# Performance work log

Measured on AMD Instinct MI355X. Metric: run time of the kernel, lower is better.

## Reference

```python
import jax, jax.numpy as jnp
import numpy as np

B, T, C, H = 8, 2048, 768, 64  # batch, block_size, n_embd, head_size

def setup_inputs() -> dict:
    key = jax.random.key(0)
    kx, kk, kq, kv = jax.random.split(key, 4)
    x = jax.random.normal(kx, (B, T, C), dtype=jnp.float32)
    Wk = jax.random.normal(kk, (C, H), dtype=jnp.float32) * (C ** -0.5)
    Wq = jax.random.normal(kq, (C, H), dtype=jnp.float32) * (C ** -0.5)
    Wv = jax.random.normal(kv, (C, H), dtype=jnp.float32) * (C ** -0.5)
    return {"x": x, "Wk": Wk, "Wq": Wq, "Wv": Wv}

def reference(x, Wk, Wq, Wv):
    # single causal self-attention head (dropout in eval mode = identity)
    k = jnp.einsum('btc,ch->bth', x, Wk)  # [B,T,H]
    q = jnp.einsum('btc,ch->bth', x, Wq)
    v = jnp.einsum('btc,ch->bth', x, Wv)
    scale = jnp.asarray(k.shape[-1], x.dtype) ** -0.5
    wei = jnp.einsum('bth,bsh->bts', q, k) * scale  # [B,T,T]
    t = x.shape[1]
    causal = jnp.tril(jnp.ones((t, t), dtype=bool))
    wei = jnp.where(causal[None, :, :], wei, jnp.asarray(-jnp.inf, wei.dtype))
    wei = jax.nn.softmax(wei, axis=-1)
    out = jnp.einsum('bts,bsh->bth', wei, v)  # [B,T,H]
    return out
```

## Files before the change

### kernel.cpp

```cpp
#include <hip/hip_runtime.h>
#include <hip/hip_bf16.h>

typedef __attribute__((ext_vector_type(8))) short short8;
typedef __attribute__((ext_vector_type(4))) float f32x4;

#define B_  8
#define T_  2048
#define C_  768
#define H_  64
#define M_  (B_ * T_)

#define GLDS16(g, l) __builtin_amdgcn_global_load_lds(                        \
    (const __attribute__((address_space(1))) void*)(g),                       \
    (__attribute__((address_space(3))) void*)(l), 16, 0, 0)

static __device__ __forceinline__ unsigned short f2bf(float f) {
    __hip_bfloat16 h = __float2bfloat16(f);
    return *reinterpret_cast<unsigned short*>(&h);
}

static __device__ __forceinline__ short8 make_frag(const unsigned short* p0, const unsigned short* p1) {
    const ushort4 a = *reinterpret_cast<const ushort4*>(p0);
    const ushort4 b = *reinterpret_cast<const ushort4*>(p1);
    short8 r;
    r[0] = (short)a.x; r[1] = (short)a.y; r[2] = (short)a.z; r[3] = (short)a.w;
    r[4] = (short)b.x; r[5] = (short)b.y; r[6] = (short)b.z; r[7] = (short)b.w;
    return r;
}

static __device__ __forceinline__ int swz(int row, int u) {
    return row * 64 + ((((u) >> 3) ^ (row & 7)) << 3) + (u & 7);
}

static __device__ __forceinline__ int fragoff(int k) {
    const int half = k >> 5;
    const int kk   = k & 31;
    const int c    = half * 4 + ((kk >> 2) & 3);
    const int p    = (kk & 3) + ((kk & 16) >> 2);
    return c * 8 + p;
}

#define LOG2E_SCALE 0.18033688011112042f

__global__ __launch_bounds__(256) void prep_w(
    const float* __restrict__ Wq, const float* __restrict__ Wk, const float* __restrict__ Wv,
    unsigned short* __restrict__ Wt) {

    const int t   = threadIdx.x;
    const int mat = blockIdx.x / 48;
    const int kb  = blockIdx.x % 48;
    const int h   = t & 63;
    const int k0  = (kb * 4 + (t >> 6)) * 4;

    const float* Ws = (mat == 0) ? Wq : (mat == 1) ? Wk : Wv;
    const float sc  = (mat == 0) ? LOG2E_SCALE : 1.f;
    ushort4 o;
    o.x = f2bf(Ws[(size_t)(k0 + 0) * H_ + h] * sc);
    o.y = f2bf(Ws[(size_t)(k0 + 1) * H_ + h] * sc);
    o.z = f2bf(Ws[(size_t)(k0 + 2) * H_ + h] * sc);
    o.w = f2bf(Ws[(size_t)(k0 + 3) * H_ + h] * sc);
    *reinterpret_cast<ushort4*>(&Wt[(size_t)(mat * 64 + h) * C_ + k0]) = o;
}

__global__ __launch_bounds__(256) void proj_kernel(
    const float* __restrict__ x, const unsigned short* __restrict__ Wt,
    unsigned short* __restrict__ qkv) {

    __shared__ unsigned short Als[2][8192];

    const int tid = threadIdx.x;
    const int w   = tid >> 6;
    const int l   = tid & 63;
    const int lg  = l >> 4;
    const int lc  = l & 15;
    const int row0 = blockIdx.x * 64;

    const int sr   = tid >> 2;
    const int so   = tid & 3;
    const int srt  = sr >> 4;
    const int sr15 = sr & 15;
    const int sbase = (so * 16 + (sr15 ^ so)) * 8;

    f32x4 acc[4][3];
#pragma unroll
    for (int rt = 0; rt < 4; ++rt)
#pragma unroll
        for (int ct = 0; ct < 3; ++ct) acc[rt][ct] = (f32x4)0.f;

    const unsigned short* bbase[3];
#pragma unroll
    for (int ct = 0; ct < 3; ++ct)
        bbase[ct] = Wt + (size_t)(w * 48 + ct * 16 + lc) * C_ + lg * 8;

    const float* xrow = x + (size_t)(row0 + sr) * C_ + so * 8;

    float4 fa[4][2];
#pragma unroll
    for (int jj = 0; jj < 4; ++jj) {
        fa[jj][0] = *reinterpret_cast<const float4*>(xrow + jj * 32);
        fa[jj][1] = *reinterpret_cast<const float4*>(xrow + jj * 32 + 4);
    }

#pragma unroll
    for (int c = 0; c < 6; ++c) {
#pragma unroll
        for (int jj = 0; jj < 4; ++jj) {
            short8 v;
            v[0] = (short)f2bf(fa[jj][0].x); v[1] = (short)f2bf(fa[jj][0].y);
            v[2] = (short)f2bf(fa[jj][0].z); v[3] = (short)f2bf(fa[jj][0].w);
            v[4] = (short)f2bf(fa[jj][1].x); v[5] = (short)f2bf(fa[jj][1].y);
            v[6] = (short)f2bf(fa[jj][1].z); v[7] = (short)f2bf(fa[jj][1].w);
            *reinterpret_cast<short8*>(&Als[c & 1][(srt * 4 + jj) * 512 + sbase]) = v;
        }
        if (c < 5) {
#pragma unroll
            for (int jj = 0; jj < 4; ++jj) {
                fa[jj][0] = *reinterpret_cast<const float4*>(xrow + (c + 1) * 128 + jj * 32);
                fa[jj][1] = *reinterpret_cast<const float4*>(xrow + (c + 1) * 128 + jj * 32 + 4);
            }
        }
        __syncthreads();
#pragma unroll
        for (int kk = 0; kk < 4; ++kk) {
            short8 bcur[3];
#pragma unroll
            for (int ct = 0; ct < 3; ++ct)
                bcur[ct] = *reinterpret_cast<const short8*>(bbase[ct] + c * 128 + kk * 32);
            short8 af[4];
#pragma unroll
            for (int rt = 0; rt < 4; ++rt)
                af[rt] = *reinterpret_cast<const short8*>(
                    &Als[c & 1][(rt * 4 + kk) * 512 + (lg * 16 + (lc ^ lg)) * 8]);
#pragma unroll
            for (int rt = 0; rt < 4; ++rt)
#pragma unroll
                for (int ct = 0; ct < 3; ++ct)
                    acc[rt][ct] = __builtin_amdgcn_mfma_f32_16x16x32_bf16(af[rt], bcur[ct], acc[rt][ct], 0, 0, 0);
        }
    }

    unsigned short* Qd   = qkv;
    unsigned short* Kimg = qkv + (size_t)M_ * H_;
    unsigned short* Vimg = qkv + (size_t)2 * M_ * H_;
    const size_t g12 = (size_t)blockIdx.x << 12;
#pragma unroll
    for (int ct = 0; ct < 3; ++ct) {
        const int col = w * 48 + ct * 16 + lc;
        const int mat = col >> 6;
        const int h   = col & 63;
        const int foh = fragoff(h);
#pragma unroll
        for (int rt = 0; rt < 4; ++rt)
#pragma unroll
            for (int j = 0; j < 4; ++j) {
                const int s6 = rt * 16 + lg * 4 + j;
                const unsigned short v = f2bf(acc[rt][ct][j]);
                if (mat == 0)      Qd[(size_t)(row0 + s6) * H_ + h] = v;
                else if (mat == 1) Kimg[g12 + swz(s6, foh)] = v;
                else               Vimg[g12 + swz(h, fragoff(s6))] = v;
            }
    }
}

#define SEG_FLOATS 4224

template<int SEG>
static __device__ __forceinline__ int segs_per_batch() { return SEG == 32 ? 32 : 80; }

template<int SEG>
static __device__ __forceinline__ void decode_seg(int r, int& qt, int& seg) {
    if (SEG == 32) { qt = r; seg = 0; return; }
    if (r < 8)       { qt = r;                seg = 0; }
    else if (r < 24) { qt = 8  + (r - 8) / 2; seg = (r - 8) & 1; }
    else if (r < 48) { qt = 16 + (r - 24) / 3; seg = (r - 24) % 3; }
    else             { qt = 24 + (r - 48) / 4; seg = (r - 48) & 3; }
}

template<int SEG>
static __device__ __forceinline__ int seg_prefix(int qt) {
    if (SEG == 32) return qt;
    if (qt < 8)  return qt;
    if (qt < 16) return 8  + 2 * (qt - 8);
    if (qt < 24) return 24 + 3 * (qt - 16);
    return 48 + 4 * (qt - 24);
}

template<int SEG>
__global__ __launch_bounds__(256) void attn_partial(
    const unsigned short* __restrict__ qkv, float* __restrict__ part,
    float* __restrict__ out) {

    const int spb = segs_per_batch<SEG>();
    const int b   = blockIdx.x / spb;
    const int rr  = spb - 1 - (blockIdx.x % spb);
    int qt, seg;
    decode_seg<SEG>(rr, qt, seg);

    const int tid = threadIdx.x;
    const int w  = tid >> 6;
    const int l  = tid & 63;
    const int lg = l >> 4;
    const int lc = l & 15;

    __shared__ unsigned short Kls[2][4096];
    __shared__ unsigned short Vls[2][4096];

    const unsigned short* Qg = qkv;
    const unsigned short* Kg = qkv + (size_t)M_ * H_;
    const unsigned short* Vg = qkv + (size_t)2 * M_ * H_;

    const unsigned short* qrow = Qg + (size_t)(b * T_ + qt * 64 + w * 16 + lc) * H_;
    short8 qf[2];
#pragma unroll
    for (int ks = 0; ks < 2; ++ks)
        qf[ks] = make_frag(qrow + ks * 32 + lg * 4, qrow + ks * 32 + lg * 4 + 16);

    float mval = -1e30f, lsum = 0.f;
    f32x4 oT[4];
#pragma unroll
    for (int t = 0; t < 4; ++t) oT[t] = (f32x4)0.f;

    const int q_glob = qt * 64 + w * 16 + lc;

    const int kv_beg = seg * SEG;
    const int kv_end = min(kv_beg + SEG, qt + 1);

    const int go = w * 1024 + l * 8;

    auto stage = [&](int buf, int kv) {
        const size_t tb = ((size_t)(b * 32 + kv)) << 12;
        const unsigned short* kt = Kg + tb;
        const unsigned short* vt = Vg + tb;
        GLDS16(kt + go,       &Kls[buf][w * 1024]);
        GLDS16(kt + go + 512, &Kls[buf][w * 1024 + 512]);
        GLDS16(vt + go,       &Vls[buf][w * 1024]);
        GLDS16(vt + go + 512, &Vls[buf][w * 1024 + 512]);
    };

    stage(0, kv_beg);
    int cur = 0;

    for (int kv = kv_beg; kv < kv_end; ++kv) {
        const bool more = (kv + 1 < kv_end);
        __builtin_amdgcn_s_barrier();
        asm volatile("" ::: "memory");
        if (more) {
            stage(cur ^ 1, kv + 1);
            asm volatile("s_waitcnt vmcnt(4)" ::: "memory");
        } else {
            asm volatile("s_waitcnt vmcnt(0)" ::: "memory");
        }
        __builtin_amdgcn_s_barrier();
        asm volatile("" ::: "memory");

        const unsigned short* Kc = Kls[cur];
        const unsigned short* Vc = Vls[cur];

        f32x4 sT[4];
#pragma unroll
        for (int st = 0; st < 4; ++st) {
            f32x4 accs = (f32x4)0.f;
#pragma unroll
            for (int ks = 0; ks < 2; ++ks) {
                const short8 kf = *reinterpret_cast<const short8*>(
                    &Kc[swz(st * 16 + lc, (ks * 4 + lg) * 8)]);
                accs = __builtin_amdgcn_mfma_f32_16x16x32_bf16(kf, qf[ks], accs, 0, 0, 0);
            }
            sT[st] = accs;
        }

        float p[4][4];
#pragma unroll
        for (int st = 0; st < 4; ++st)
#pragma unroll
            for (int r = 0; r < 4; ++r)
                p[st][r] = sT[st][r];

        if (kv == qt) {
#pragma unroll
            for (int st = 0; st < 4; ++st)
#pragma unroll
                for (int r = 0; r < 4; ++r)
                    if ((kv * 64 + st * 16 + lg * 4 + r) > q_glob) p[st][r] = -1e30f;
        }

        float pm[4];
#pragma unroll
        for (int st = 0; st < 4; ++st)
            pm[st] = fmaxf(fmaxf(p[st][0], p[st][1]), fmaxf(p[st][2], p[st][3]));
        float pmax = fmaxf(fmaxf(pm[0], pm[1]), fmaxf(pm[2], pm[3]));
        pmax = fmaxf(pmax, __shfl_xor(pmax, 16));
        pmax = fmaxf(pmax, __shfl_xor(pmax, 32));

        if (!__all(pmax <= mval)) {
            const float mnew  = fmaxf(mval, pmax);
            const float alpha = exp2f(mval - mnew);
            mval = mnew;
            lsum *= alpha;
#pragma unroll
            for (int ht = 0; ht < 4; ++ht) oT[ht] *= alpha;
        }

        float ps[4];
#pragma unroll
        for (int st = 0; st < 4; ++st) {
#pragma unroll
            for (int r = 0; r < 4; ++r)
                p[st][r] = exp2f(p[st][r] - mval);
            ps[st] = (p[st][0] + p[st][1]) + (p[st][2] + p[st][3]);
        }
        float srow = (ps[0] + ps[1]) + (ps[2] + ps[3]);
        srow += __shfl_xor(srow, 16);
        srow += __shfl_xor(srow, 32);
        lsum += srow;

        short8 pb[2];
#pragma unroll
        for (int ks = 0; ks < 2; ++ks) {
#pragma unroll
            for (int r = 0; r < 4; ++r) {
                pb[ks][r]     = (short)f2bf(p[2 * ks][r]);
                pb[ks][r + 4] = (short)f2bf(p[2 * ks + 1][r]);
            }
        }

#pragma unroll
        for (int ks = 0; ks < 2; ++ks) {
#pragma unroll
            for (int ht = 0; ht < 4; ++ht) {
                const short8 vf = *reinterpret_cast<const short8*>(
                    &Vc[swz(ht * 16 + lc, (ks * 4 + lg) * 8)]);
                oT[ht] = __builtin_amdgcn_mfma_f32_16x16x32_bf16(vf, pb[ks], oT[ht], 0, 0, 0);
            }
        }
        cur ^= 1;
    }

    const int nseg = (SEG == 32) ? 1 : (qt / 8 + 1);
    if (nseg == 1) {
        const float inv = 1.f / lsum;
        float* op = out + (size_t)(b * T_ + q_glob) * H_;
#pragma unroll
        for (int ht = 0; ht < 4; ++ht) {
            f32x4 v = oT[ht] * inv;
            *reinterpret_cast<f32x4*>(&op[ht * 16 + lg * 4]) = v;
        }
    } else {
        float* base = part + (size_t)(b * spb + seg_prefix<SEG>(qt) + seg) * SEG_FLOATS;
#pragma unroll
        for (int ht = 0; ht < 4; ++ht)
            *reinterpret_cast<f32x4*>(&base[(w * 16 + lc) * 64 + ht * 16 + lg * 4]) = oT[ht];
        if (lg == 0) {
            base[4096 + w * 16 + lc] = mval;
            base[4160 + w * 16 + lc] = lsum;
        }
    }
}

__global__ __launch_bounds__(256) void attn_merge8(
    const float* __restrict__ part, float* __restrict__ out) {

    const int b  = blockIdx.x / 24;
    const int qt = 8 + blockIdx.x % 24;
    const int nseg = qt / 8 + 1;
    const float* base0 = part + (size_t)(b * 80 + seg_prefix<8>(qt)) * SEG_FLOATS;

    const int tid = threadIdx.x;
    const int row = tid >> 2;
    const int c0  = (tid & 3) * 16;

    float M = -1e30f;
    for (int s = 0; s < nseg; ++s)
        M = fmaxf(M, base0[(size_t)s * SEG_FLOATS + 4096 + row]);

    float L = 0.f;
    f32x4 acc[4];
#pragma unroll
    for (int k = 0; k < 4; ++k) acc[k] = (f32x4)0.f;

    for (int s = 0; s < nseg; ++s) {
        const float* sb = base0 + (size_t)s * SEG_FLOATS;
        const float wsc = exp2f(sb[4096 + row] - M);
        L += sb[4160 + row] * wsc;
#pragma unroll
        for (int k = 0; k < 4; ++k) {
            const f32x4 ov = *reinterpret_cast<const f32x4*>(&sb[row * 64 + c0 + 4 * k]);
            acc[k] += ov * wsc;
        }
    }
    const float inv = 1.f / L;
    float* op = out + (size_t)(b * T_ + qt * 64 + row) * H_ + c0;
#pragma unroll
    for (int k = 0; k < 4; ++k)
        *reinterpret_cast<f32x4*>(&op[4 * k]) = acc[k] * inv;
}

extern "C" void kernel_launch(void* const* d_in, const int* in_sizes, int n_in,
                              void* d_out, int out_size, void* d_ws, size_t ws_size,
                              hipStream_t stream) {
    const float* x  = (const float*)d_in[0];
    const float* Wk = (const float*)d_in[1];
    const float* Wq = (const float*)d_in[2];
    const float* Wv = (const float*)d_in[3];

    const size_t qkvB = (size_t)3 * M_ * H_ * 2;
    const size_t WtB  = (size_t)3 * H_ * C_ * 2;
    unsigned short* qkv = (unsigned short*)d_ws;
    unsigned short* Wt  = (unsigned short*)((char*)d_ws + qkvB);
    float* part = (float*)((char*)d_ws + qkvB + WtB);
    float* out  = (float*)d_out;

    prep_w<<<dim3(144), dim3(256), 0, stream>>>(Wq, Wk, Wv, Wt);
    proj_kernel<<<dim3(M_ / 64), dim3(256), 0, stream>>>(x, Wt, qkv);

    const size_t need8 = qkvB + WtB + (size_t)(B_ * 80) * SEG_FLOATS * 4;
    if (ws_size >= need8) {
        attn_partial<8><<<dim3(B_ * 80), dim3(256), 0, stream>>>(qkv, part, out);
        attn_merge8<<<dim3(B_ * 24), dim3(256), 0, stream>>>(part, out);
    } else {
        attn_partial<32><<<dim3(B_ * 32), dim3(256), 0, stream>>>(qkv, part, out);
    }
}
```

Measured before the change: 56.12 us.

## Process KV tiles in pairs and stage QKV projection output through LDS

```diff
diff --git a/kernel.cpp b/kernel.cpp
--- a/kernel.cpp
+++ b/kernel.cpp
@@ -139,10 +139,8 @@
         }
     }
 
-    unsigned short* Qd   = qkv;
-    unsigned short* Kimg = qkv + (size_t)M_ * H_;
-    unsigned short* Vimg = qkv + (size_t)2 * M_ * H_;
-    const size_t g12 = (size_t)blockIdx.x << 12;
+    __syncthreads();
+    unsigned short* Ls = &Als[0][0];
 #pragma unroll
     for (int ct = 0; ct < 3; ++ct) {
         const int col = w * 48 + ct * 16 + lc;
@@ -155,10 +153,27 @@
             for (int j = 0; j < 4; ++j) {
                 const int s6 = rt * 16 + lg * 4 + j;
                 const unsigned short v = f2bf(acc[rt][ct][j]);
-                if (mat == 0)      Qd[(size_t)(row0 + s6) * H_ + h] = v;
-                else if (mat == 1) Kimg[g12 + swz(s6, foh)] = v;
-                else               Vimg[g12 + swz(h, fragoff(s6))] = v;
-            }
+                if (mat == 0)      Ls[s6 * 64 + h] = v;
+                else if (mat == 1) Ls[4096 + swz(s6, foh)] = v;
+                else               Ls[8192 + swz(h, fragoff(s6))] = v;
+            }
+    }
+    __syncthreads();
+
+    unsigned short* Qd   = qkv;
+    unsigned short* Kimg = qkv + (size_t)M_ * H_;
+    unsigned short* Vimg = qkv + (size_t)2 * M_ * H_;
+    const size_t g12 = (size_t)blockIdx.x << 12;
+    const int o = tid * 8;
+#pragma unroll
+    for (int s = 0; s < 2; ++s) {
+        const int off = s * 2048 + o;
+        *reinterpret_cast<short8*>(&Qd[(size_t)row0 * 64 + off]) =
+            *reinterpret_cast<const short8*>(&Ls[off]);
+        *reinterpret_cast<short8*>(&Kimg[g12 + off]) =
+            *reinterpret_cast<const short8*>(&Ls[4096 + off]);
+        *reinterpret_cast<short8*>(&Vimg[g12 + off]) =
+            *reinterpret_cast<const short8*>(&Ls[8192 + off]);
     }
 }
 
@@ -202,8 +217,8 @@
     const int lg = l >> 4;
     const int lc = l & 15;
 
-    __shared__ unsigned short Kls[2][4096];
-    __shared__ unsigned short Vls[2][4096];
+    __shared__ unsigned short Kls[2][2][4096];
+    __shared__ unsigned short Vls[2][2][4096];
 
     const unsigned short* Qg = qkv;
     const unsigned short* Kg = qkv + (size_t)M_ * H_;
@@ -224,71 +239,89 @@
 
     const int kv_beg = seg * SEG;
     const int kv_end = min(kv_beg + SEG, qt + 1);
+    const int npair  = (kv_end - kv_beg + 1) >> 1;
 
     const int go = w * 1024 + l * 8;
 
-    auto stage = [&](int buf, int kv) {
-        const size_t tb = ((size_t)(b * 32 + kv)) << 12;
-        const unsigned short* kt = Kg + tb;
-        const unsigned short* vt = Vg + tb;
-        GLDS16(kt + go,       &Kls[buf][w * 1024]);
-        GLDS16(kt + go + 512, &Kls[buf][w * 1024 + 512]);
-        GLDS16(vt + go,       &Vls[buf][w * 1024]);
-        GLDS16(vt + go + 512, &Vls[buf][w * 1024 + 512]);
+    auto stage = [&](int buf, int pi) {
+        const size_t tb0 = ((size_t)(b * 32 + kv_beg + 2 * pi)) << 12;
+        const size_t tb1 = tb0 + 4096;
+        GLDS16(Kg + tb0 + go,       &Kls[buf][0][w * 1024]);
+        GLDS16(Kg + tb0 + go + 512, &Kls[buf][0][w * 1024 + 512]);
+        GLDS16(Kg + tb1 + go,       &Kls[buf][1][w * 1024]);
+        GLDS16(Kg + tb1 + go + 512, &Kls[buf][1][w * 1024 + 512]);
+        GLDS16(Vg + tb0 + go,       &Vls[buf][0][w * 1024]);
+        GLDS16(Vg + tb0 + go + 512, &Vls[buf][0][w * 1024 + 512]);
+        GLDS16(Vg + tb1 + go,       &Vls[buf][1][w * 1024]);
+        GLDS16(Vg + tb1 + go + 512, &Vls[buf][1][w * 1024 + 512]);
     };
 
-    stage(0, kv_beg);
+    stage(0, 0);
     int cur = 0;
 
-    for (int kv = kv_beg; kv < kv_end; ++kv) {
-        const bool more = (kv + 1 < kv_end);
+    for (int pi = 0; pi < npair; ++pi) {
+        const int t0 = kv_beg + 2 * pi;
         __builtin_amdgcn_s_barrier();
         asm volatile("" ::: "memory");
-        if (more) {
-            stage(cur ^ 1, kv + 1);
-            asm volatile("s_waitcnt vmcnt(4)" ::: "memory");
+        if (pi + 1 < npair) {
+            stage(cur ^ 1, pi + 1);
+            asm volatile("s_waitcnt vmcnt(8)" ::: "memory");
         } else {
             asm volatile("s_waitcnt vmcnt(0)" ::: "memory");
         }
         __builtin_amdgcn_s_barrier();
         asm volatile("" ::: "memory");
 
-        const unsigned short* Kc = Kls[cur];
-        const unsigned short* Vc = Vls[cur];
-
-        f32x4 sT[4];
-#pragma unroll
-        for (int st = 0; st < 4; ++st) {
-            f32x4 accs = (f32x4)0.f;
-#pragma unroll
-            for (int ks = 0; ks < 2; ++ks) {
-                const short8 kf = *reinterpret_cast<const short8*>(
-                    &Kc[swz(st * 16 + lc, (ks * 4 + lg) * 8)]);
-                accs = __builtin_amdgcn_mfma_f32_16x16x32_bf16(kf, qf[ks], accs, 0, 0, 0);
-            }
-            sT[st] = accs;
-        }
-
-        float p[4][4];
-#pragma unroll
-        for (int st = 0; st < 4; ++st)
-#pragma unroll
-            for (int r = 0; r < 4; ++r)
-                p[st][r] = sT[st][r];
-
-        if (kv == qt) {
+        f32x4 sT[2][4];
+#pragma unroll
+        for (int t = 0; t < 2; ++t) {
+            const unsigned short* Kc = Kls[cur][t];
+#pragma unroll
+            for (int st = 0; st < 4; ++st) {
+                f32x4 accs = (f32x4)0.f;
+#pragma unroll
+                for (int ks = 0; ks < 2; ++ks) {
+                    const short8 kf = *reinterpret_cast<const short8*>(
+                        &Kc[swz(st * 16 + lc, (ks * 4 + lg) * 8)]);
+                    accs = __builtin_amdgcn_mfma_f32_16x16x32_bf16(kf, qf[ks], accs, 0, 0, 0);
+                }
+                sT[t][st] = accs;
+            }
+        }
+
+        float p[2][4][4];
+#pragma unroll
+        for (int t = 0; t < 2; ++t)
 #pragma unroll
             for (int st = 0; st < 4; ++st)
 #pragma unroll
                 for (int r = 0; r < 4; ++r)
-                    if ((kv * 64 + st * 16 + lg * 4 + r) > q_glob) p[st][r] = -1e30f;
-        }
-
-        float pm[4];
-#pragma unroll
-        for (int st = 0; st < 4; ++st)
-            pm[st] = fmaxf(fmaxf(p[st][0], p[st][1]), fmaxf(p[st][2], p[st][3]));
-        float pmax = fmaxf(fmaxf(pm[0], pm[1]), fmaxf(pm[2], pm[3]));
+                    p[t][st][r] = sT[t][st][r];
+
+        if (t0 == qt) {
+#pragma unroll
+            for (int st = 0; st < 4; ++st)
+#pragma unroll
+                for (int r = 0; r < 4; ++r)
+                    if ((t0 * 64 + st * 16 + lg * 4 + r) > q_glob) p[0][st][r] = -1e30f;
+        }
+        if (t0 + 1 >= qt) {
+#pragma unroll
+            for (int st = 0; st < 4; ++st)
+#pragma unroll
+                for (int r = 0; r < 4; ++r)
+                    if (((t0 + 1) * 64 + st * 16 + lg * 4 + r) > q_glob) p[1][st][r] = -1e30f;
+        }
+
+        float pm[2][4];
+#pragma unroll
+        for (int t = 0; t < 2; ++t)
+#pragma unroll
+            for (int st = 0; st < 4; ++st)
+                pm[t][st] = fmaxf(fmaxf(p[t][st][0], p[t][st][1]),
+                                  fmaxf(p[t][st][2], p[t][st][3]));
+        float pmax = fmaxf(fmaxf(fmaxf(pm[0][0], pm[0][1]), fmaxf(pm[0][2], pm[0][3])),
+                           fmaxf(fmaxf(pm[1][0], pm[1][1]), fmaxf(pm[1][2], pm[1][3])));
         pmax = fmaxf(pmax, __shfl_xor(pmax, 16));
         pmax = fmaxf(pmax, __shfl_xor(pmax, 32));
 
@@ -301,36 +334,43 @@
             for (int ht = 0; ht < 4; ++ht) oT[ht] *= alpha;
         }
 
-        float ps[4];
-#pragma unroll
-        for (int st = 0; st < 4; ++st) {
-#pragma unroll
-            for (int r = 0; r < 4; ++r)
-                p[st][r] = exp2f(p[st][r] - mval);
-            ps[st] = (p[st][0] + p[st][1]) + (p[st][2] + p[st][3]);
-        }
-        float srow = (ps[0] + ps[1]) + (ps[2] + ps[3]);
+        float srow = 0.f;
+#pragma unroll
+        for (int t = 0; t < 2; ++t) {
+            float ps[4];
+#pragma unroll
+            for (int st = 0; st < 4; ++st) {
+#pragma unroll
+                for (int r = 0; r < 4; ++r)
+                    p[t][st][r] = exp2f(p[t][st][r] - mval);
+                ps[st] = (p[t][st][0] + p[t][st][1]) + (p[t][st][2] + p[t][st][3]);
+            }
+            srow += (ps[0] + ps[1]) + (ps[2] + ps[3]);
+        }
         srow += __shfl_xor(srow, 16);
         srow += __shfl_xor(srow, 32);
         lsum += srow;
 
-        short8 pb[2];
-#pragma unroll
-        for (int ks = 0; ks < 2; ++ks) {
-#pragma unroll
-            for (int r = 0; r < 4; ++r) {
-                pb[ks][r]     = (short)f2bf(p[2 * ks][r]);
-                pb[ks][r + 4] = (short)f2bf(p[2 * ks + 1][r]);
-            }
-        }
-
-#pragma unroll
-        for (int ks = 0; ks < 2; ++ks) {
-#pragma unroll
-            for (int ht = 0; ht < 4; ++ht) {
-                const short8 vf = *reinterpret_cast<const short8*>(
-                    &Vc[swz(ht * 16 + lc, (ks * 4 + lg) * 8)]);
-                oT[ht] = __builtin_amdgcn_mfma_f32_16x16x32_bf16(vf, pb[ks], oT[ht], 0, 0, 0);
+#pragma unroll
+        for (int t = 0; t < 2; ++t) {
+            short8 pb[2];
+#pragma unroll
+            for (int ks = 0; ks < 2; ++ks) {
+#pragma unroll
+                for (int r = 0; r < 4; ++r) {
+                    pb[ks][r]     = (short)f2bf(p[t][2 * ks][r]);
+                    pb[ks][r + 4] = (short)f2bf(p[t][2 * ks + 1][r]);
+                }
+            }
+            const unsigned short* Vc = Vls[cur][t];
+#pragma unroll
+            for (int ks = 0; ks < 2; ++ks) {
+#pragma unroll
+                for (int ht = 0; ht < 4; ++ht) {
+                    const short8 vf = *reinterpret_cast<const short8*>(
+                        &Vc[swz(ht * 16 + lc, (ks * 4 + lg) * 8)]);
+                    oT[ht] = __builtin_amdgcn_mfma_f32_16x16x32_bf16(vf, pb[ks], oT[ht], 0, 0, 0);
+                }
             }
         }
         cur ^= 1;
```

Result: no change. 56.98 us (+1.5%).

## Stage QKV epilogue through LDS and triple-buffer K/V loads in attention

Applied to the files above, without the earlier changes.

```diff
diff --git a/kernel.cpp b/kernel.cpp
--- a/kernel.cpp
+++ b/kernel.cpp
@@ -139,10 +139,8 @@
         }
     }
 
-    unsigned short* Qd   = qkv;
-    unsigned short* Kimg = qkv + (size_t)M_ * H_;
-    unsigned short* Vimg = qkv + (size_t)2 * M_ * H_;
-    const size_t g12 = (size_t)blockIdx.x << 12;
+    __syncthreads();
+    unsigned short* Ls = &Als[0][0];
 #pragma unroll
     for (int ct = 0; ct < 3; ++ct) {
         const int col = w * 48 + ct * 16 + lc;
@@ -155,10 +153,27 @@
             for (int j = 0; j < 4; ++j) {
                 const int s6 = rt * 16 + lg * 4 + j;
                 const unsigned short v = f2bf(acc[rt][ct][j]);
-                if (mat == 0)      Qd[(size_t)(row0 + s6) * H_ + h] = v;
-                else if (mat == 1) Kimg[g12 + swz(s6, foh)] = v;
-                else               Vimg[g12 + swz(h, fragoff(s6))] = v;
+                if (mat == 0)      Ls[s6 * 64 + h] = v;
+                else if (mat == 1) Ls[4096 + swz(s6, foh)] = v;
+                else               Ls[8192 + swz(h, fragoff(s6))] = v;
             }
+    }
+    __syncthreads();
+
+    unsigned short* Qd   = qkv;
+    unsigned short* Kimg = qkv + (size_t)M_ * H_;
+    unsigned short* Vimg = qkv + (size_t)2 * M_ * H_;
+    const size_t g12 = (size_t)blockIdx.x << 12;
+    const int o = tid * 8;
+#pragma unroll
+    for (int s = 0; s < 2; ++s) {
+        const int off = s * 2048 + o;
+        *reinterpret_cast<short8*>(&Qd[(size_t)row0 * 64 + off]) =
+            *reinterpret_cast<const short8*>(&Ls[off]);
+        *reinterpret_cast<short8*>(&Kimg[g12 + off]) =
+            *reinterpret_cast<const short8*>(&Ls[4096 + off]);
+        *reinterpret_cast<short8*>(&Vimg[g12 + off]) =
+            *reinterpret_cast<const short8*>(&Ls[8192 + off]);
     }
 }
 
@@ -202,8 +217,8 @@
     const int lg = l >> 4;
     const int lc = l & 15;
 
-    __shared__ unsigned short Kls[2][4096];
-    __shared__ unsigned short Vls[2][4096];
+    __shared__ unsigned short Kls[3][4096];
+    __shared__ unsigned short Vls[3][4096];
 
     const unsigned short* Qg = qkv;
     const unsigned short* Kg = qkv + (size_t)M_ * H_;
@@ -224,6 +239,7 @@
 
     const int kv_beg = seg * SEG;
     const int kv_end = min(kv_beg + SEG, qt + 1);
+    const int n      = kv_end - kv_beg;
 
     const int go = w * 1024 + l * 8;
 
@@ -238,14 +254,16 @@
     };
 
     stage(0, kv_beg);
-    int cur = 0;
-
-    for (int kv = kv_beg; kv < kv_end; ++kv) {
-        const bool more = (kv + 1 < kv_end);
+    if (n > 1) stage(1, kv_beg + 1);
+
+    int b0 = 0;
+    for (int i = 0; i < n; ++i) {
         __builtin_amdgcn_s_barrier();
         asm volatile("" ::: "memory");
-        if (more) {
-            stage(cur ^ 1, kv + 1);
+        if (i + 2 < n) {
+            stage((b0 + 2) % 3, kv_beg + i + 2);
+            asm volatile("s_waitcnt vmcnt(8)" ::: "memory");
+        } else if (i + 1 < n) {
             asm volatile("s_waitcnt vmcnt(4)" ::: "memory");
         } else {
             asm volatile("s_waitcnt vmcnt(0)" ::: "memory");
@@ -253,8 +271,9 @@
         __builtin_amdgcn_s_barrier();
         asm volatile("" ::: "memory");
 
-        const unsigned short* Kc = Kls[cur];
-        const unsigned short* Vc = Vls[cur];
+        const int kv = kv_beg + i;
+        const unsigned short* Kc = Kls[b0];
+        const unsigned short* Vc = Vls[b0];
 
         f32x4 sT[4];
 #pragma unroll
@@ -333,7 +352,7 @@
                 oT[ht] = __builtin_amdgcn_mfma_f32_16x16x32_bf16(vf, pb[ks], oT[ht], 0, 0, 0);
             }
         }
-        cur ^= 1;
+        b0 = (b0 == 2) ? 0 : b0 + 1;
     }
 
     const int nseg = (SEG == 32) ? 1 : (qt / 8 + 1);
```

Measured after the change: 57.03 us. Within noise of the previous version (+1.6%).
